# Kernel optimization log

Measured on AMD Instinct MI355X. Metric: run time of the kernel, lower is better.

Reference implementation:

```python
import jax, jax.numpy as jnp
import numpy as np

N, FEAT, D, K, L, H, NCLS = 4096, 512, 64, 100, 3, 8, 2
EPS = 1e-15

def _ln(x, g, b, eps=1e-6):
    m = x.mean(-1, keepdims=True)
    v = x.var(-1, keepdims=True)
    return (x - m) * jax.lax.rsqrt(v + eps) * g + b


def setup_inputs():
    key = jax.random.key(0)
    ks = jax.random.split(key, 12)
    w = lambda k, shape: jax.random.normal(k, shape, jnp.float32) * 0.02
    return {
        "node_feat": jax.random.normal(ks[0], (1, N, FEAT), jnp.float32),
        "adj": jax.random.uniform(ks[1], (1, N, N), jnp.float32),
        "conv_w": w(ks[2], (FEAT, D)), "conv_b": jnp.zeros((D,), jnp.float32),
        "bn_g": jnp.ones((D,), jnp.float32), "bn_b": jnp.zeros((D,), jnp.float32),
        "pool_w": w(ks[3], (D, K)), "pool_b": jnp.zeros((K,), jnp.float32),
        "cls_token": jnp.zeros((1, 1, D), jnp.float32),
        "ln1_g": jnp.ones((L, D), jnp.float32), "ln1_b": jnp.zeros((L, D), jnp.float32),
        "qkv_w": w(ks[4], (L, D, 3 * D)), "qkv_b": jnp.zeros((L, 3 * D), jnp.float32),
        "proj_w": w(ks[5], (L, D, D)), "proj_b": jnp.zeros((L, D), jnp.float32),
        "ln2_g": jnp.ones((L, D), jnp.float32), "ln2_b": jnp.zeros((L, D), jnp.float32),
        "fc1_w": w(ks[6], (L, D, 4 * D)), "fc1_b": jnp.zeros((L, 4 * D), jnp.float32),
        "fc2_w": w(ks[7], (L, 4 * D, D)), "fc2_b": jnp.zeros((L, D), jnp.float32),
        "norm_g": jnp.ones((D,), jnp.float32), "norm_b": jnp.zeros((D,), jnp.float32),
        "head_w": w(ks[8], (D, NCLS)), "head_b": jnp.zeros((NCLS,), jnp.float32),
    }


def _forward(node_feat, adj, conv_w, conv_b, bn_g, bn_b, pool_w, pool_b, cls_token,
             ln1_g, ln1_b, qkv_w, qkv_b, proj_w, proj_b, ln2_g, ln2_b,
             fc1_w, fc1_b, fc2_w, fc2_b, norm_g, norm_b, head_w, head_b):
    x = node_feat  # mask is all ones -> X = mask*X is a no-op
    # --- GCNBlock: propagate + self loop + linear + BatchNorm(train stats) + L2 norm ---
    y = jnp.matmul(adj, x) + x                 # [1,N,F]
    y = y @ conv_w + conv_b                    # [1,N,D]
    m = y.mean(axis=(0, 1))
    v = y.var(axis=(0, 1))
    y = (y - m) * jax.lax.rsqrt(v + 1e-5) * bn_g + bn_b
    y = y / jnp.maximum(jnp.linalg.norm(y, axis=2, keepdims=True), 1e-12)
    # --- cluster assignment ---
    s = jax.nn.softmax(y @ pool_w + pool_b, axis=-1)   # [1,N,K]
    # --- dense_mincut_pool ---
    out = jnp.einsum('bnk,bnd->bkd', s, y)             # [1,K,D]
    sa = s[0].T @ adj[0]                               # [K,N] (the torch.sparse.mm)
    out_adj = (sa @ s[0])[None]                        # [1,K,K]
    mincut_num = jnp.trace(out_adj, axis1=1, axis2=2)  # [1]
    d_flat = adj.sum(-1)                               # [1,N] degrees
    # trace(S^T diag(d) S) = sum_i d_i * ||s_i||^2
    mincut_den = jnp.sum(d_flat[0] * jnp.sum(s[0] ** 2, axis=-1))[None]
    mincut_loss = jnp.mean(-(mincut_num / mincut_den))
    ss = jnp.einsum('bnk,bnl->bkl', s, s)
    i_s = jnp.eye(K, dtype=ss.dtype)
    ortho_loss = jnp.mean(jnp.linalg.norm(
        ss / jnp.linalg.norm(ss, axis=(-1, -2), keepdims=True) - i_s / jnp.linalg.norm(i_s),
        axis=(-1, -2)))
    ind = jnp.arange(K)
    out_adj = out_adj.at[:, ind, ind].set(0.0)
    dd = jnp.sqrt(out_adj.sum(-1))[:, None] + EPS      # [1,1,K]
    out_adj = out_adj / dd / jnp.swapaxes(dd, 1, 2)    # (returned by pool; unused downstream)
    # --- transformer over [cls] + K cluster tokens ---
    t = jnp.concatenate([jnp.broadcast_to(cls_token, (1, 1, D)), out], axis=1)  # [1,K+1,D]
    hd = D // H
    scale = hd ** -0.5
    for l in range(L):
        h = _ln(t, ln1_g[l], ln1_b[l])
        qkv = h @ qkv_w[l] + qkv_b[l]
        q, k, vv = jnp.split(qkv, 3, axis=-1)
        sp = lambda a: a.reshape(1, -1, H, hd).transpose(0, 2, 1, 3)
        q, k, vv = sp(q), sp(k), sp(vv)
        att = jax.nn.softmax(jnp.einsum('bhqd,bhkd->bhqk', q, k) * scale, axis=-1)
        o = jnp.einsum('bhqk,bhkd->bhqd', att, vv).transpose(0, 2, 1, 3).reshape(1, -1, D)
        t = t + (o @ proj_w[l] + proj_b[l])
        h = _ln(t, ln2_g[l], ln2_b[l])
        t = t + (jax.nn.gelu(h @ fc1_w[l] + fc1_b[l], approximate=False) @ fc2_w[l] + fc2_b[l])
    t = _ln(t, norm_g, norm_b)
    logits = t[:, 0] @ head_w + head_b                 # [1,NCLS]
    return logits, mincut_loss, ortho_loss


def reference(node_feat, adj, conv_w, conv_b, bn_g, bn_b, pool_w, pool_b, cls_token,
              ln1_g, ln1_b, qkv_w, qkv_b, proj_w, proj_b, ln2_g, ln2_b,
              fc1_w, fc1_b, fc2_w, fc2_b, norm_g, norm_b, head_w, head_b):
    return _forward(node_feat, adj, conv_w, conv_b, bn_g, bn_b, pool_w, pool_b, cls_token,
                    ln1_g, ln1_b, qkv_w, qkv_b, proj_w, proj_b, ln2_g, ln2_b,
                    fc1_w, fc1_b, fc2_w, fc2_b, norm_g, norm_b, head_w, head_b)
```

## Files before the change

kernel.cpp:

```cpp
#include <hip/hip_runtime.h>
#include <hip/hip_bf16.h>
#include <math.h>

#define NN   4096
#define FEAT 512
#define DIM  64
#define KC   100
#define LL   3

#define OFF_DFLAT   0
#define OFF_CHSUM   4096
#define OFF_CHSQ    4160
#define OFF_CTR     4224
#define ZERO_FLOATS 4240
#define OFF_XW      4240
#define OFF_YPART   (OFF_XW + NN*DIM)
#define OFF_GPART   (OFF_YPART + 8*NN*DIM)
#define OFF_Y0      (OFF_GPART + 64*128*192)
#define OFF_QKV     (OFF_Y0 + NN*DIM)
#define OFF_SS      (OFF_QKV + 2*101*192)
#define OFF_DENP    (OFF_SS + KC*KC)
#define OFF_NUMP    (OFF_DENP + 1024)
#define OFF_SB16    (OFF_NUMP + 1024)
#define OFF_STB16   (OFF_SB16 + NN*128/2)
#define OFF_YNT16   (OFF_STB16 + NN*128/2)
#define OFF_XWT16   (OFF_YNT16 + NN*DIM/2)

typedef __attribute__((ext_vector_type(8))) short bfrag;
typedef __attribute__((ext_vector_type(4))) float ffrag;

__device__ __forceinline__ unsigned short f2bf(float f) {
    union { float f; unsigned u; } v; v.f = f;
    return (unsigned short)((v.u + 0x7FFFu + ((v.u >> 16) & 1u)) >> 16);
}
__device__ __forceinline__ float bf2f(unsigned short u) {
    union { unsigned u; float f; } v; v.u = (unsigned)u << 16; return v.f;
}
__device__ __forceinline__ unsigned int pk2(float a, float b) {
    __hip_bfloat162 h = __float22bfloat162_rn(make_float2(a, b));
    return *(unsigned int*)&h;
}

__device__ __forceinline__ float wsum(float v) {
#pragma unroll
    for (int o = 32; o > 0; o >>= 1) v += __shfl_xor(v, o, 64);
    return v;
}
__device__ __forceinline__ float wmax(float v) {
#pragma unroll
    for (int o = 32; o > 0; o >>= 1) v = fmaxf(v, __shfl_xor(v, o, 64));
    return v;
}
__device__ __forceinline__ float hsum32(float v) {
#pragma unroll
    for (int o = 16; o > 0; o >>= 1) v += __shfl_xor(v, o, 64);
    return v;
}
__device__ __forceinline__ float hmax32(float v) {
#pragma unroll
    for (int o = 16; o > 0; o >>= 1) v = fmaxf(v, __shfl_xor(v, o, 64));
    return v;
}

__device__ __forceinline__ unsigned rlx_load(const unsigned* p) {
    return __hip_atomic_load(p, __ATOMIC_RELAXED, __HIP_MEMORY_SCOPE_AGENT);
}
__device__ __forceinline__ void rel_add(unsigned* p) {
    __hip_atomic_fetch_add(p, 1u, __ATOMIC_RELEASE, __HIP_MEMORY_SCOPE_AGENT);
}
template <int SLP>
__device__ __forceinline__ void wait_ge(const unsigned* c, unsigned tgt) {
    while (rlx_load(c) < tgt) __builtin_amdgcn_s_sleep(SLP);
    __builtin_amdgcn_fence(__ATOMIC_ACQUIRE, "agent");
}
__device__ __forceinline__ void bar() {
    asm volatile("s_waitcnt lgkmcnt(0)" ::: "memory");
    __builtin_amdgcn_s_barrier();
}
__device__ __forceinline__ void gbar(unsigned* c, unsigned tgt) {
    __syncthreads();
    if (threadIdx.x == 0) {
        rel_add(c);
        wait_ge<4>(c, tgt);
    }
    bar();
}

__global__ __launch_bounds__(256) void xwk(const float* __restrict__ x,
                                           const float* __restrict__ B,
                                           float* __restrict__ xw,
                                           unsigned short* __restrict__ xwT,
                                           float* __restrict__ zws) {
    __shared__ float a_sh[16 * 68];
    __shared__ float b_sh[64 * 68];
    __shared__ unsigned short tl[64 * 17];
    const int t = threadIdx.x, rb = blockIdx.x;
    if (rb < 17) {
        const int zi = rb * 256 + t;
        if (zi < ZERO_FLOATS) zws[zi] = 0.f;
    }
    const int r = t >> 4, cg = (t & 15) * 4;
    float4 acc = make_float4(0.f, 0.f, 0.f, 0.f);
    for (int kt = 0; kt < FEAT; kt += 64) {
        *(float4*)&a_sh[(t >> 4) * 68 + (t & 15) * 4] =
            *(const float4*)(x + (size_t)(rb * 16 + (t >> 4)) * FEAT + kt + (t & 15) * 4);
#pragma unroll
        for (int p = 0; p < 4; ++p) {
            const int idx = t + 256 * p;
            const int kr = idx >> 4, c4 = (idx & 15) * 4;
            *(float4*)&b_sh[kr * 68 + c4] = *(const float4*)(B + (size_t)(kt + kr) * DIM + c4);
        }
        __syncthreads();
#pragma unroll 8
        for (int k = 0; k < 64; ++k) {
            const float av = a_sh[r * 68 + k];
            const float4 bv = *(float4*)&b_sh[k * 68 + cg];
            acc.x += av * bv.x; acc.y += av * bv.y;
            acc.z += av * bv.z; acc.w += av * bv.w;
        }
        __syncthreads();
    }
    *(float4*)&xw[(size_t)(rb * 16 + r) * DIM + cg] = acc;
    tl[(cg + 0) * 17 + r] = f2bf(acc.x);
    tl[(cg + 1) * 17 + r] = f2bf(acc.y);
    tl[(cg + 2) * 17 + r] = f2bf(acc.z);
    tl[(cg + 3) * 17 + r] = f2bf(acc.w);
    __syncthreads();
    const int d = t >> 2, c = (t & 3) * 4;
    ushort4 o;
    o.x = tl[d * 17 + c + 0]; o.y = tl[d * 17 + c + 1];
    o.z = tl[d * 17 + c + 2]; o.w = tl[d * 17 + c + 3];
    *(ushort4*)(xwT + (size_t)d * NN + rb * 16 + c) = o;
}

__global__ __launch_bounds__(256) void gemmA(const float* __restrict__ adj,
                                             const unsigned short* __restrict__ xwT,
                                             float* __restrict__ ypart,
                                             float* __restrict__ dflat) {
    __shared__ __align__(16) unsigned short a_sh[32 * 72];
    __shared__ __align__(16) unsigned short b_sh[64 * 72];
    const int t  = threadIdx.x;
    const int rb = blockIdx.x;
    const int k0 = blockIdx.y * 512;
    const int w = t >> 6, lane = t & 63;
    const int m = lane & 15, q = lane >> 4;
    const int ih = w & 1, jh = w >> 1;
    const int srow = t >> 3, sq = t & 7;
    const int bn = t >> 2, bc = t & 3;
    ffrag acc[2];
    acc[0] = (ffrag){0.f, 0.f, 0.f, 0.f};
    acc[1] = (ffrag){0.f, 0.f, 0.f, 0.f};
    float dacc = 0.f;
    const float* abase = adj + (size_t)(rb * 32 + srow) * NN + k0;
    const unsigned short* bbase = xwT + (size_t)bn * NN + k0;
    for (int kt = 0; kt < 512; kt += 64) {
#pragma unroll
        for (int k = 0; k < 2; ++k) {
            const int p = sq + 8 * k;
            const float4 v = *(const float4*)(abase + kt + 4 * p);
            dacc += v.x + v.y + v.z + v.w;
            *(uint2*)(a_sh + srow * 72 + 4 * p) = make_uint2(pk2(v.x, v.y), pk2(v.z, v.w));
        }
#pragma unroll
        for (int k = 0; k < 2; ++k) {
            const int c2 = bc + 4 * k;
            *(bfrag*)(b_sh + bn * 72 + c2 * 8) = *(const bfrag*)(bbase + kt + c2 * 8);
        }
        __syncthreads();
#pragma unroll
        for (int ks = 0; ks < 2; ++ks) {
            const bfrag af = *(const bfrag*)(a_sh + (ih * 16 + m) * 72 + ks * 32 + q * 8);
#pragma unroll
            for (int jj = 0; jj < 2; ++jj) {
                const bfrag bf = *(const bfrag*)(b_sh + ((jh * 2 + jj) * 16 + m) * 72 + ks * 32 + q * 8);
                acc[jj] = __builtin_amdgcn_mfma_f32_16x16x32_bf16(af, bf, acc[jj], 0, 0, 0);
            }
        }
        __syncthreads();
    }
    float* op = ypart + (size_t)blockIdx.y * NN * DIM;
#pragma unroll
    for (int jj = 0; jj < 2; ++jj)
#pragma unroll
        for (int r = 0; r < 4; ++r)
            op[(size_t)(rb * 32 + ih * 16 + q * 4 + r) * DIM + jh * 32 + jj * 16 + m] = acc[jj][r];
    dacc += __shfl_down(dacc, 1, 64);
    dacc += __shfl_down(dacc, 2, 64);
    dacc += __shfl_down(dacc, 4, 64);
    if (sq == 0) atomicAdd(&dflat[rb * 32 + srow], dacc);
}

__global__ __launch_bounds__(256) void bnstat(const float* __restrict__ ypart,
                                              const float* __restrict__ xw,
                                              const float* __restrict__ conv_b,
                                              float* __restrict__ Y0,
                                              float* __restrict__ chsum,
                                              float* __restrict__ chsq) {
    __shared__ float ssum[64], ssq[64];
    const int t = threadIdx.x;
    if (t < 64) { ssum[t] = 0.f; ssq[t] = 0.f; }
    __syncthreads();
    const int tid = blockIdx.x * 256 + t;
    const size_t e = (size_t)tid * 4;
    const int c0 = (int)(e & 63);
    float4 v = *(const float4*)(xw + e);
#pragma unroll
    for (int s = 0; s < 8; ++s) {
        const float4 u = *(const float4*)(ypart + (size_t)s * NN * DIM + e);
        v.x += u.x; v.y += u.y; v.z += u.z; v.w += u.w;
    }
    const float4 b = *(const float4*)(conv_b + c0);
    v.x += b.x; v.y += b.y; v.z += b.z; v.w += b.w;
    *(float4*)(Y0 + e) = v;
    atomicAdd(&ssum[c0 + 0], v.x); atomicAdd(&ssum[c0 + 1], v.y);
    atomicAdd(&ssum[c0 + 2], v.z); atomicAdd(&ssum[c0 + 3], v.w);
    atomicAdd(&ssq[c0 + 0], v.x * v.x); atomicAdd(&ssq[c0 + 1], v.y * v.y);
    atomicAdd(&ssq[c0 + 2], v.z * v.z); atomicAdd(&ssq[c0 + 3], v.w * v.w);
    __syncthreads();
    if (t < 64) { atomicAdd(&chsum[t], ssum[t]); atomicAdd(&chsq[t], ssq[t]); }
}

__global__ __launch_bounds__(256) void rowsk(const float* __restrict__ Y0,
                                             const float* __restrict__ bn_g,
                                             const float* __restrict__ bn_b,
                                             const float* __restrict__ chsum,
                                             const float* __restrict__ chsq,
                                             const float* __restrict__ pool_w,
                                             const float* __restrict__ pool_b,
                                             const float* __restrict__ dflat,
                                             unsigned short* __restrict__ YnT,
                                             unsigned short* __restrict__ Sb16,
                                             unsigned short* __restrict__ ST,
                                             float* __restrict__ denp) {
    __shared__ float scale_sh[64], shift_sh[64];
    __shared__ float yn_sh[4][64];
    __shared__ float4 pw4[16 * 104];
    __shared__ unsigned short sb_sh[4][128];
    __shared__ float denw[4];
    const int t = threadIdx.x;
    if (t < 64) {
        const float mn  = chsum[t] * (1.f / 4096.f);
        const float var = chsq[t] * (1.f / 4096.f) - mn * mn;
        const float sc  = bn_g[t] * rsqrtf(var + 1e-5f);
        scale_sh[t] = sc;
        shift_sh[t] = bn_b[t] - mn * sc;
    }
    for (int idx = t; idx < 16 * KC; idx += 256) {
        const int dq = idx / KC, k = idx - dq * KC;
        pw4[dq * 104 + k] = make_float4(pool_w[(4 * dq + 0) * KC + k],
                                        pool_w[(4 * dq + 1) * KC + k],
                                        pool_w[(4 * dq + 2) * KC + k],
                                        pool_w[(4 * dq + 3) * KC + k]);
    }
    __syncthreads();
    const int w = t >> 6, lane = t & 63;
    const int row = blockIdx.x * 4 + w;
    float v = Y0[(size_t)row * 64 + lane] * scale_sh[lane] + shift_sh[lane];
    const float nrm = fmaxf(sqrtf(wsum(v * v)), 1e-12f);
    const float yn = v / nrm;
    yn_sh[w][lane] = yn;
    const bool v2 = (lane + 64) < KC;
    const int j2 = v2 ? (lane + 64) : 0;
    float L1 = pool_b[lane];
    float L2 = pool_b[j2];
    __syncthreads();
#pragma unroll
    for (int dq = 0; dq < 16; ++dq) {
        const float4 yv = *(const float4*)&yn_sh[w][4 * dq];
        const float4 w1 = pw4[dq * 104 + lane];
        L1 += yv.x * w1.x + yv.y * w1.y + yv.z * w1.z + yv.w * w1.w;
        const float4 w2 = pw4[dq * 104 + j2];
        L2 += yv.x * w2.x + yv.y * w2.y + yv.z * w2.z + yv.w * w2.w;
    }
    const float mx = wmax(fmaxf(L1, v2 ? L2 : -1e30f));
    const float e1 = expf(L1 - mx);
    const float e2 = v2 ? expf(L2 - mx) : 0.f;
    const float inv = 1.f / wsum(e1 + e2);
    const float s1 = e1 * inv, s2 = e2 * inv;
    const unsigned short b1 = f2bf(s1), b2 = f2bf(s2);
    Sb16[(size_t)row * 128 + lane] = b1;
    Sb16[(size_t)row * 128 + 64 + lane] = b2;
    sb_sh[w][lane] = b1;
    sb_sh[w][64 + lane] = b2;
    const float c = wsum(s1 * s1 + s2 * s2);
    if (lane == 0) denw[w] = dflat[row] * c;
    __syncthreads();
    if (t < 64) {
        ushort4 o;
        o.x = f2bf(yn_sh[0][t]); o.y = f2bf(yn_sh[1][t]);
        o.z = f2bf(yn_sh[2][t]); o.w = f2bf(yn_sh[3][t]);
        *(ushort4*)(YnT + (size_t)t * NN + blockIdx.x * 4) = o;
    } else if (t < 192) {
        const int c2 = t - 64;
        ushort4 o;
        o.x = sb_sh[0][c2]; o.y = sb_sh[1][c2];
        o.z = sb_sh[2][c2]; o.w = sb_sh[3][c2];
        *(ushort4*)(ST + (size_t)c2 * NN + blockIdx.x * 4) = o;
    } else if (t == 192) {
        denp[blockIdx.x] = denw[0] + denw[1] + denw[2] + denw[3];
    }
}

__global__ __launch_bounds__(512) void xform(
        const float* __restrict__ adj,
        const unsigned short* __restrict__ ST,
        const unsigned short* __restrict__ Sb16,
        const unsigned short* __restrict__ YnT,
        float* __restrict__ gpart,
        const float* __restrict__ cls,
        float* __restrict__ ssb,
        float* __restrict__ qkvb,
        const float* __restrict__ g1, const float* __restrict__ b1,
        const float* __restrict__ qw, const float* __restrict__ qb,
        const float* __restrict__ pw, const float* __restrict__ pb,
        const float* __restrict__ g2, const float* __restrict__ b2,
        const float* __restrict__ w1, const float* __restrict__ bb1,
        const float* __restrict__ w2, const float* __restrict__ bb2,
        const float* __restrict__ ng, const float* __restrict__ nb,
        const float* __restrict__ hw, const float* __restrict__ hb,
        const float* __restrict__ denp, float* __restrict__ nump,
        unsigned* __restrict__ ctr,
        float* __restrict__ out) {
    __shared__ __align__(16) float big[13332];
    __shared__ float scsh[8 * 104];
    __shared__ __align__(16) float partf[1056];
    __shared__ float q_l[64], osh[64], h2sh[64], h1sh[64], toksh[64], gsh[256];
    __shared__ float redw8[8];
    float (*part)[132] = (float(*)[132])partf;
    const int t = threadIdx.x, b = blockIdx.x;

    if (b < 101) {
        float4 rqkv[6];
        {
            const float4* s4 = (const float4*)qw;
#pragma unroll
            for (int p = 0; p < 6; ++p) rqkv[p] = s4[t + 512 * p];
        }
        if (b == 0) {
            if (t < 64) toksh[t] = cls[t];
        } else {
            if (t == 0) wait_ge<2>(&ctr[3], 64u);
            bar();
            const int row = b - 1;
            if (t < 384) {
                const int col = t % 192, sg = t / 192;
                float v = 0.f;
                const float* gp = gpart + (size_t)row * 192 + col + (size_t)sg * 32 * 24576;
                for (int s = 0; s < 32; ++s) v += gp[(size_t)s * 24576];
                partf[sg * 192 + col] = v;
            }
            bar();
            if (t < 192) {
                const float v = partf[t] + partf[192 + t];
                if (t < 64) toksh[t] = v;
                else if (t < 164) ssb[row * 100 + (t - 64)] = v;
            }
        }
        bar();
        if (t < 64) {
            const float x = toksh[t];
            const float m = wsum(x) * (1.f / 64.f);
            const float var = wsum(x * x) * (1.f / 64.f) - m * m;
            h1sh[t] = (x - m) * rsqrtf(var + 1e-6f) * g1[t] + b1[t];
        }
        bar();
        for (int l = 0; l < LL; ++l) {
            float* qk = qkvb + (size_t)(l & 1) * (101 * 192);
#pragma unroll
            for (int p = 0; p < 6; ++p) ((float4*)big)[t + 512 * p] = rqkv[p];
            bar();
            if (t < 384) {
                const int o = t % 192, grp = t / 192;
                float a = 0.f;
#pragma unroll 8
                for (int e = grp * 32; e < grp * 32 + 32; ++e)
                    a += h1sh[e] * big[e * 192 + o];
                partf[grp * 192 + o] = a;
            }
            bar();
            if (t < 192)
                qk[b * 192 + t] = qb[l * 192 + t] + partf[t] + partf[192 + t];
            gbar(&ctr[l], 101u);
            float4 rkv[7], rq, rpw[2], rw1a[4];
#pragma unroll
            for (int p = 0; p < 7; ++p) {
                const int idx = t + 512 * p;
                if (idx < 3232)
                    rkv[p] = *(const float4*)(qk + (idx >> 5) * 192 + 64 + (idx & 31) * 4);
            }
            if (t < 16) rq = *(const float4*)(qk + b * 192 + t * 4);
#pragma unroll
            for (int p = 0; p < 2; ++p)
                rpw[p] = ((const float4*)(pw + (size_t)l * 4096))[t + 512 * p];
#pragma unroll
            for (int p = 0; p < 4; ++p) {
                const int idx = t + 512 * p;
                rw1a[p] = *(const float4*)(w1 + (size_t)l * 16384 + (idx >> 5) * 256 + (idx & 31) * 4);
            }
            float t_old = 0.f;
            if (t < 64) t_old = toksh[t];
#pragma unroll
            for (int p = 0; p < 7; ++p) {
                const int idx = t + 512 * p;
                if (idx < 3232) {
                    const int k = idx >> 5, c = idx & 31;
                    *(float4*)&big[k * 132 + c * 4] = rkv[p];
                }
            }
            if (t < 16) *(float4*)&q_l[t * 4] = rq;
            bar();
            const float scale = 0.35355339059327373f;
#pragma unroll
            for (int p = 0; p < 2; ++p) {
                const int idx = t + 512 * p;
                if (idx < 808) {
                    const int h = idx / 101, k = idx - h * 101;
                    float s = 0.f;
#pragma unroll
                    for (int d = 0; d < 8; ++d)
                        s += q_l[h * 8 + d] * big[k * 132 + h * 8 + d];
                    scsh[h * 104 + k] = s * scale;
                }
            }
            bar();
            if (t < 256) {
                const int w = t >> 6;
                const int h = w * 2 + ((t >> 5) & 1);
                const int lft = t & 31;
                float v[4];
#pragma unroll
                for (int g = 0; g < 4; ++g) {
                    const int k = lft + 32 * g;
                    v[g] = (k < 101) ? scsh[h * 104 + k] : -1e30f;
                }
                float mm = fmaxf(fmaxf(v[0], v[1]), fmaxf(v[2], v[3]));
                mm = hmax32(mm);
                float s = 0.f;
#pragma unroll
                for (int g = 0; g < 4; ++g) { v[g] = expf(v[g] - mm); s += v[g]; }
                s = hsum32(s);
                const float inv = 1.f / s;
#pragma unroll
                for (int g = 0; g < 4; ++g) {
                    const int k = lft + 32 * g;
                    if (k < 101) scsh[h * 104 + k] = v[g] * inv;
                }
            }
            bar();
            {
                const int o = t & 63, grp = t >> 6;
                float po = 0.f;
                for (int k = grp; k < 101; k += 8)
                    po += scsh[(o >> 3) * 104 + k] * big[k * 132 + 64 + o];
                part[grp][o] = po;
            }
            bar();
            if (t < 64)
                osh[t] = part[0][t] + part[1][t] + part[2][t] + part[3][t]
                       + part[4][t] + part[5][t] + part[6][t] + part[7][t];
            float4 rw1b[4], rw2a[4], rw2b[4];
#pragma unroll
            for (int p = 0; p < 4; ++p) {
                const int idx = t + 512 * p;
                rw1b[p] = *(const float4*)(w1 + (size_t)l * 16384 + (idx >> 5) * 256 + 128 + (idx & 31) * 4);
                rw2a[p] = ((const float4*)(w2 + (size_t)l * 16384))[idx];
                rw2b[p] = ((const float4*)(w2 + (size_t)l * 16384 + 8192))[idx];
            }
            bar();
#pragma unroll
            for (int p = 0; p < 2; ++p) ((float4*)big)[t + 512 * p] = rpw[p];
            bar();
            {
                const int o = t & 63, grp = t >> 6;
                float pp = 0.f;
#pragma unroll
                for (int e = grp * 8; e < grp * 8 + 8; ++e)
                    pp += osh[e] * big[e * 64 + o];
                part[grp][o] = pp;
            }
            bar();
            float t1 = 0.f;
            if (t < 64) {
                float pr = pb[l * 64 + t];
#pragma unroll
                for (int g = 0; g < 8; ++g) pr += part[g][t];
                t1 = t_old + pr;
                const float m = wsum(t1) * (1.f / 64.f);
                const float var = wsum(t1 * t1) * (1.f / 64.f) - m * m;
                h2sh[t] = (t1 - m) * rsqrtf(var + 1e-6f) * g2[l * 64 + t] + b2[l * 64 + t];
            }
            bar();
#pragma unroll
            for (int p = 0; p < 4; ++p) {
                const int idx = t + 512 * p;
                *(float4*)&big[(idx >> 5) * 128 + (idx & 31) * 4] = rw1a[p];
            }
            bar();
            {
                const int o = t & 127, grp = t >> 7;
                float pa = 0.f;
#pragma unroll
                for (int e = grp * 16; e < grp * 16 + 16; ++e)
                    pa += h2sh[e] * big[e * 128 + o];
                part[grp][o] = pa;
            }
            bar();
            if (t < 128) {
                float a = bb1[l * 256 + t]
                        + part[0][t] + part[1][t] + part[2][t] + part[3][t];
                gsh[t] = 0.5f * a * (1.f + erff(a * 0.70710678118654752f));
            }
            bar();
#pragma unroll
            for (int p = 0; p < 4; ++p) {
                const int idx = t + 512 * p;
                *(float4*)&big[(idx >> 5) * 128 + (idx & 31) * 4] = rw1b[p];
            }
            bar();
            {
                const int o = t & 127, grp = t >> 7;
                float pa = 0.f;
#pragma unroll
                for (int e = grp * 16; e < grp * 16 + 16; ++e)
                    pa += h2sh[e] * big[e * 128 + o];
                part[grp][o] = pa;
            }
            bar();
            if (t < 128) {
                float a = bb1[l * 256 + 128 + t]
                        + part[0][t] + part[1][t] + part[2][t] + part[3][t];
                gsh[128 + t] = 0.5f * a * (1.f + erff(a * 0.70710678118654752f));
            }
            bar();
            float a2p = 0.f;
#pragma unroll
            for (int p = 0; p < 4; ++p) ((float4*)big)[t + 512 * p] = rw2a[p];
            bar();
            {
                const int o = t & 63, grp = t >> 6;
#pragma unroll
                for (int er = grp * 16; er < grp * 16 + 16; ++er)
                    a2p += gsh[er] * big[er * 64 + o];
            }
            bar();
#pragma unroll
            for (int p = 0; p < 4; ++p) ((float4*)big)[t + 512 * p] = rw2b[p];
            bar();
            {
                const int o = t & 63, grp = t >> 6;
#pragma unroll
                for (int er = grp * 16; er < grp * 16 + 16; ++er)
                    a2p += gsh[128 + er] * big[er * 64 + o];
            }
            if (l < 2) {
                const float4* s4 = (const float4*)(qw + (size_t)(l + 1) * 12288);
#pragma unroll
                for (int p = 0; p < 6; ++p) rqkv[p] = s4[t + 512 * p];
            }
            bar();
            {
                const int o = t & 63, grp = t >> 6;
                part[grp][o] = a2p;
            }
            bar();
            if (t < 64) {
                float a2 = bb2[l * 64 + t];
#pragma unroll
                for (int g = 0; g < 8; ++g) a2 += part[g][t];
                const float tn = t1 + a2;
                toksh[t] = tn;
                if (l < 2) {
                    const float m = wsum(tn) * (1.f / 64.f);
                    const float var = wsum(tn * tn) * (1.f / 64.f) - m * m;
                    h1sh[t] = (tn - m) * rsqrtf(var + 1e-6f) * g1[(l + 1) * 64 + t]
                              + b1[(l + 1) * 64 + t];
                }
            }
            bar();
        }
        if (b == 0) {
            if (t < 64) {
                const float x = toksh[t];
                const float m = wsum(x) * (1.f / 64.f);
                const float var = wsum(x * x) * (1.f / 64.f) - m * m;
                h1sh[t] = (x - m) * rsqrtf(var + 1e-6f) * ng[t] + nb[t];
            }
            if (t == 0) wait_ge<8>(&ctr[4], 155u);
            __syncthreads();
            float* red = partf;
            red[t] = denp[t] + denp[t + 512];
            __syncthreads();
            for (int s = 256; s > 0; s >>= 1) { if (t < s) red[t] += red[t + s]; __syncthreads(); }
            if (t == 0) q_l[0] = red[0];
            __syncthreads();
            red[t] = nump[t] + nump[t + 512];
            __syncthreads();
            for (int s = 256; s > 0; s >>= 1) { if (t < s) red[t] += red[t + s]; __syncthreads(); }
            if (t == 0) q_l[1] = red[0];
            __syncthreads();
            if (t < 2) {
                float a = hb[t];
                for (int d = 0; d < 64; ++d) a += h1sh[d] * hw[d * 2 + t];
                out[t] = a;
            }
            if (t == 2) out[2] = -(q_l[1] / q_l[0]);
            float s1 = 0.f;
            for (int idx = t; idx < KC * KC; idx += 512) { const float v = ssb[idx]; s1 += v * v; }
            __syncthreads();
            red[t] = s1;
            __syncthreads();
            for (int s = 256; s > 0; s >>= 1) { if (t < s) red[t] += red[t + s]; __syncthreads(); }
            if (t == 0) q_l[2] = sqrtf(red[0]);
            __syncthreads();
            const float inv = 1.f / q_l[2];
            float s2 = 0.f;
            for (int idx = t; idx < KC * KC; idx += 512) {
                float v = ssb[idx] * inv;
                if (idx % 101 == 0) v -= 0.1f;
                s2 += v * v;
            }
            __syncthreads();
            red[t] = s2;
            __syncthreads();
            for (int s = 256; s > 0; s >>= 1) { if (t < s) red[t] += red[t + s]; __syncthreads(); }
            if (t == 0) out[3] = sqrtf(red[0]);
        }
    } else {
        const int wb = b - 101;
        const int w = t >> 6, lane = t & 63;
        const int m = lane & 15, q = lane >> 4;
        if (wb < 64) {
            unsigned short* a_sh = (unsigned short*)big;
            unsigned short* b_sh = (unsigned short*)big + 128 * 72;
            const int k0 = wb * 64;
            const int n0 = t >> 3, c8 = (t & 7) * 8;
#pragma unroll
            for (int p = 0; p < 2; ++p) {
                const int n = n0 + 64 * p;
                *(bfrag*)(a_sh + n * 72 + c8) = *(const bfrag*)(ST + (size_t)n * NN + k0 + c8);
            }
#pragma unroll
            for (int p = 0; p < 3; ++p) {
                const int n = n0 + 64 * p;
                const unsigned short* src = (n < 64) ? (YnT + (size_t)n * NN + k0 + c8)
                                                     : (ST + (size_t)(n - 64) * NN + k0 + c8);
                *(bfrag*)(b_sh + n * 72 + c8) = *(const bfrag*)src;
            }
            __syncthreads();
            ffrag acc[12];
#pragma unroll
            for (int j = 0; j < 12; ++j) acc[j] = (ffrag){0.f, 0.f, 0.f, 0.f};
#pragma unroll
            for (int ks = 0; ks < 2; ++ks) {
                const bfrag af = *(const bfrag*)(a_sh + (w * 16 + m) * 72 + ks * 32 + q * 8);
#pragma unroll
                for (int j = 0; j < 12; ++j) {
                    const bfrag bf = *(const bfrag*)(b_sh + (j * 16 + m) * 72 + ks * 32 + q * 8);
                    acc[j] = __builtin_amdgcn_mfma_f32_16x16x32_bf16(af, bf, acc[j], 0, 0, 0);
                }
            }
            float* op = gpart + (size_t)wb * 128 * 192;
#pragma unroll
            for (int j = 0; j < 12; ++j)
#pragma unroll
                for (int r = 0; r < 4; ++r)
                    op[(size_t)(w * 16 + q * 4 + r) * 192 + j * 16 + m] = acc[j][r];
            __syncthreads();
            if (t == 0) rel_add(&ctr[3]);
        }
        unsigned short* a_sh = (unsigned short*)big;
        unsigned short* s_sh = (unsigned short*)big + 32 * 72;
        const int rh = w & 1, ch = w >> 1;
        const int srow = t >> 4, sq4 = (t & 15) * 4;
        const int sn = t >> 2, scq = t & 3;
        for (int tile = wb; tile < 1024; tile += 155) {
            const int rb = tile & 127;
            const int k0 = (tile >> 7) * 512;
            ffrag acc[2];
            acc[0] = (ffrag){0.f, 0.f, 0.f, 0.f};
            acc[1] = (ffrag){0.f, 0.f, 0.f, 0.f};
            const float* abase = adj + (size_t)(rb * 32 + srow) * NN + k0;
            const unsigned short* sbase = ST + (size_t)sn * NN + k0;
            for (int kt = 0; kt < 512; kt += 64) {
                {
                    const float4 v = *(const float4*)(abase + kt + sq4);
                    *(uint2*)(a_sh + srow * 72 + sq4) = make_uint2(pk2(v.x, v.y), pk2(v.z, v.w));
                }
#pragma unroll
                for (int k = 0; k < 2; ++k) {
                    const int c2 = scq + 4 * k;
                    *(bfrag*)(s_sh + sn * 72 + c2 * 8) = *(const bfrag*)(sbase + kt + c2 * 8);
                }
                __syncthreads();
#pragma unroll
                for (int ks = 0; ks < 2; ++ks) {
                    const bfrag af = *(const bfrag*)(a_sh + (rh * 16 + m) * 72 + ks * 32 + q * 8);
#pragma unroll
                    for (int j = 0; j < 2; ++j) {
                        const bfrag bf = *(const bfrag*)(s_sh + ((ch * 2 + j) * 16 + m) * 72 + ks * 32 + q * 8);
                        acc[j] = __builtin_amdgcn_mfma_f32_16x16x32_bf16(af, bf, acc[j], 0, 0, 0);
                    }
                }
                __syncthreads();
            }
            float local = 0.f;
#pragma unroll
            for (int j = 0; j < 2; ++j)
#pragma unroll
                for (int r = 0; r < 4; ++r) {
                    const int row = rb * 32 + rh * 16 + q * 4 + r;
                    const int col = ch * 32 + j * 16 + m;
                    local += acc[j][r] * bf2f(Sb16[(size_t)row * 128 + col]);
                }
            local = wsum(local);
            if (lane == 0) redw8[w] = local;
            __syncthreads();
            if (t == 0) {
                float s = 0.f;
#pragma unroll
                for (int k = 0; k < 8; ++k) s += redw8[k];
                nump[(tile >> 7) * 128 + rb] = s;
            }
            __syncthreads();
        }
        __syncthreads();
        if (t == 0) rel_add(&ctr[4]);
    }
}

extern "C" void kernel_launch(void* const* d_in, const int* in_sizes, int n_in,
                              void* d_out, int out_size, void* d_ws, size_t ws_size,
                              hipStream_t stream) {
    (void)in_sizes; (void)n_in; (void)out_size; (void)ws_size;
    const float* x      = (const float*)d_in[0];
    const float* adj    = (const float*)d_in[1];
    const float* conv_w = (const float*)d_in[2];
    const float* conv_b = (const float*)d_in[3];
    const float* bn_g   = (const float*)d_in[4];
    const float* bn_b   = (const float*)d_in[5];
    const float* pool_w = (const float*)d_in[6];
    const float* pool_b = (const float*)d_in[7];
    const float* cls    = (const float*)d_in[8];
    const float* ln1_g  = (const float*)d_in[9];
    const float* ln1_b  = (const float*)d_in[10];
    const float* qkv_w  = (const float*)d_in[11];
    const float* qkv_b  = (const float*)d_in[12];
    const float* proj_w = (const float*)d_in[13];
    const float* proj_b = (const float*)d_in[14];
    const float* ln2_g  = (const float*)d_in[15];
    const float* ln2_b  = (const float*)d_in[16];
    const float* fc1_w  = (const float*)d_in[17];
    const float* fc1_b  = (const float*)d_in[18];
    const float* fc2_w  = (const float*)d_in[19];
    const float* fc2_b  = (const float*)d_in[20];
    const float* norm_g = (const float*)d_in[21];
    const float* norm_b = (const float*)d_in[22];
    const float* head_w = (const float*)d_in[23];
    const float* head_b = (const float*)d_in[24];
    float* ws  = (float*)d_ws;
    float* out = (float*)d_out;
    unsigned short* Sb16  = (unsigned short*)(ws + OFF_SB16);
    unsigned short* STb16 = (unsigned short*)(ws + OFF_STB16);
    unsigned short* YnT16 = (unsigned short*)(ws + OFF_YNT16);
    unsigned short* xwT16 = (unsigned short*)(ws + OFF_XWT16);

    xwk<<<256, 256, 0, stream>>>(x, conv_w, ws + OFF_XW, xwT16, ws);
    gemmA<<<dim3(128, 8), 256, 0, stream>>>(adj, xwT16, ws + OFF_YPART, ws + OFF_DFLAT);
    bnstat<<<256, 256, 0, stream>>>(ws + OFF_YPART, ws + OFF_XW, conv_b,
                                    ws + OFF_Y0, ws + OFF_CHSUM, ws + OFF_CHSQ);
    rowsk<<<1024, 256, 0, stream>>>(ws + OFF_Y0, bn_g, bn_b, ws + OFF_CHSUM, ws + OFF_CHSQ,
                                    pool_w, pool_b, ws + OFF_DFLAT,
                                    YnT16, Sb16, STb16, ws + OFF_DENP);
    xform<<<256, 512, 0, stream>>>(adj, STb16, Sb16, YnT16, ws + OFF_GPART, cls,
                                   ws + OFF_SS, ws + OFF_QKV,
                                   ln1_g, ln1_b, qkv_w, qkv_b, proj_w, proj_b,
                                   ln2_g, ln2_b, fc1_w, fc1_b, fc2_w, fc2_b,
                                   norm_g, norm_b, head_w, head_b,
                                   ws + OFF_DENP, ws + OFF_NUMP,
                                   (unsigned*)(ws + OFF_CTR), out);
}
```

Baseline: 290.3 us.

## Software-pipeline adj/ST tile loads and reschedule weight prefetches in xform

Register double-buffering is added to the adj·S tile loop: the next k-slice of adj and ST is loaded while the current slice is in LDS and feeding the MFMAs. Transformer-layer weight prefetches (proj, fc1, fc2, next qkv) are moved closer to where they are used, which cuts peak register pressure, and one barrier in the fc2 phase is dropped. Launch bounds are set to one block per SM, some __syncthreads are replaced with a cheaper LDS-only barrier, and an extra vmcnt wait is added after the grid-barrier spin. The trade-off is less prefetch distance for the weights and possible race risk from the removed barriers.

After: 281.1 us. 1.03x faster.

```diff
diff --git a/kernel.cpp b/kernel.cpp
--- a/kernel.cpp
+++ b/kernel.cpp
@@ -72,6 +72,7 @@
 __device__ __forceinline__ void wait_ge(const unsigned* c, unsigned tgt) {
     while (rlx_load(c) < tgt) __builtin_amdgcn_s_sleep(SLP);
     __builtin_amdgcn_fence(__ATOMIC_ACQUIRE, "agent");
+    asm volatile("s_waitcnt vmcnt(0)" ::: "memory");
 }
 __device__ __forceinline__ void bar() {
     asm volatile("s_waitcnt lgkmcnt(0)" ::: "memory");
@@ -301,7 +302,7 @@
     }
 }
 
-__global__ __launch_bounds__(512) void xform(
+__global__ __launch_bounds__(512, 1) void xform(
         const float* __restrict__ adj,
         const unsigned short* __restrict__ ST,
         const unsigned short* __restrict__ Sb16,
@@ -381,7 +382,7 @@
             if (t < 192)
                 qk[b * 192 + t] = qb[l * 192 + t] + partf[t] + partf[192 + t];
             gbar(&ctr[l], 101u);
-            float4 rkv[7], rq, rpw[2], rw1a[4];
+            float4 rkv[7], rq;
 #pragma unroll
             for (int p = 0; p < 7; ++p) {
                 const int idx = t + 512 * p;
@@ -389,14 +390,6 @@
                     rkv[p] = *(const float4*)(qk + (idx >> 5) * 192 + 64 + (idx & 31) * 4);
             }
             if (t < 16) rq = *(const float4*)(qk + b * 192 + t * 4);
-#pragma unroll
-            for (int p = 0; p < 2; ++p)
-                rpw[p] = ((const float4*)(pw + (size_t)l * 4096))[t + 512 * p];
-#pragma unroll
-            for (int p = 0; p < 4; ++p) {
-                const int idx = t + 512 * p;
-                rw1a[p] = *(const float4*)(w1 + (size_t)l * 16384 + (idx >> 5) * 256 + (idx & 31) * 4);
-            }
             float t_old = 0.f;
             if (t < 64) t_old = toksh[t];
 #pragma unroll
@@ -408,6 +401,10 @@
                 }
             }
             if (t < 16) *(float4*)&q_l[t * 4] = rq;
+            float4 rpw[2];
+#pragma unroll
+            for (int p = 0; p < 2; ++p)
+                rpw[p] = ((const float4*)(pw + (size_t)l * 4096))[t + 512 * p];
             bar();
             const float scale = 0.35355339059327373f;
 #pragma unroll
@@ -458,13 +455,11 @@
             if (t < 64)
                 osh[t] = part[0][t] + part[1][t] + part[2][t] + part[3][t]
                        + part[4][t] + part[5][t] + part[6][t] + part[7][t];
-            float4 rw1b[4], rw2a[4], rw2b[4];
+            float4 rw1a[4];
 #pragma unroll
             for (int p = 0; p < 4; ++p) {
                 const int idx = t + 512 * p;
-                rw1b[p] = *(const float4*)(w1 + (size_t)l * 16384 + (idx >> 5) * 256 + 128 + (idx & 31) * 4);
-                rw2a[p] = ((const float4*)(w2 + (size_t)l * 16384))[idx];
-                rw2b[p] = ((const float4*)(w2 + (size_t)l * 16384 + 8192))[idx];
+                rw1a[p] = *(const float4*)(w1 + (size_t)l * 16384 + (idx >> 5) * 256 + (idx & 31) * 4);
             }
             bar();
 #pragma unroll
@@ -489,6 +484,12 @@
                 const float var = wsum(t1 * t1) * (1.f / 64.f) - m * m;
                 h2sh[t] = (t1 - m) * rsqrtf(var + 1e-6f) * g2[l * 64 + t] + b2[l * 64 + t];
             }
+            float4 rw1b[4];
+#pragma unroll
+            for (int p = 0; p < 4; ++p) {
+                const int idx = t + 512 * p;
+                rw1b[p] = *(const float4*)(w1 + (size_t)l * 16384 + (idx >> 5) * 256 + 128 + (idx & 31) * 4);
+            }
             bar();
 #pragma unroll
             for (int p = 0; p < 4; ++p) {
@@ -510,6 +511,10 @@
                         + part[0][t] + part[1][t] + part[2][t] + part[3][t];
                 gsh[t] = 0.5f * a * (1.f + erff(a * 0.70710678118654752f));
             }
+            float4 rw2a[4];
+#pragma unroll
+            for (int p = 0; p < 4; ++p)
+                rw2a[p] = ((const float4*)(w2 + (size_t)l * 16384))[t + 512 * p];
             bar();
 #pragma unroll
             for (int p = 0; p < 4; ++p) {
@@ -531,6 +536,10 @@
                         + part[0][t] + part[1][t] + part[2][t] + part[3][t];
                 gsh[128 + t] = 0.5f * a * (1.f + erff(a * 0.70710678118654752f));
             }
+            float4 rw2b[4];
+#pragma unroll
+            for (int p = 0; p < 4; ++p)
+                rw2b[p] = ((const float4*)(w2 + (size_t)l * 16384 + 8192))[t + 512 * p];
             bar();
             float a2p = 0.f;
 #pragma unroll
@@ -542,6 +551,11 @@
                 for (int er = grp * 16; er < grp * 16 + 16; ++er)
                     a2p += gsh[er] * big[er * 64 + o];
             }
+            if (l < 2) {
+                const float4* s4 = (const float4*)(qw + (size_t)(l + 1) * 12288);
+#pragma unroll
+                for (int p = 0; p < 6; ++p) rqkv[p] = s4[t + 512 * p];
+            }
             bar();
 #pragma unroll
             for (int p = 0; p < 4; ++p) ((float4*)big)[t + 512 * p] = rw2b[p];
@@ -552,12 +566,6 @@
                 for (int er = grp * 16; er < grp * 16 + 16; ++er)
                     a2p += gsh[128 + er] * big[er * 64 + o];
             }
-            if (l < 2) {
-                const float4* s4 = (const float4*)(qw + (size_t)(l + 1) * 12288);
-#pragma unroll
-                for (int p = 0; p < 6; ++p) rqkv[p] = s4[t + 512 * p];
-            }
-            bar();
             {
                 const int o = t & 63, grp = t >> 6;
                 part[grp][o] = a2p;
@@ -681,17 +689,20 @@
             acc[1] = (ffrag){0.f, 0.f, 0.f, 0.f};
             const float* abase = adj + (size_t)(rb * 32 + srow) * NN + k0;
             const unsigned short* sbase = ST + (size_t)sn * NN + k0;
+            float4 av = *(const float4*)(abase + sq4);
+            bfrag sv0 = *(const bfrag*)(sbase + scq * 8);
+            bfrag sv1 = *(const bfrag*)(sbase + (scq + 4) * 8);
+#pragma unroll
             for (int kt = 0; kt < 512; kt += 64) {
-                {
-                    const float4 v = *(const float4*)(abase + kt + sq4);
-                    *(uint2*)(a_sh + srow * 72 + sq4) = make_uint2(pk2(v.x, v.y), pk2(v.z, v.w));
-                }
-#pragma unroll
-                for (int k = 0; k < 2; ++k) {
-                    const int c2 = scq + 4 * k;
-                    *(bfrag*)(s_sh + sn * 72 + c2 * 8) = *(const bfrag*)(sbase + kt + c2 * 8);
-                }
-                __syncthreads();
+                *(uint2*)(a_sh + srow * 72 + sq4) = make_uint2(pk2(av.x, av.y), pk2(av.z, av.w));
+                *(bfrag*)(s_sh + sn * 72 + scq * 8) = sv0;
+                *(bfrag*)(s_sh + sn * 72 + (scq + 4) * 8) = sv1;
+                if (kt + 64 < 512) {
+                    av  = *(const float4*)(abase + kt + 64 + sq4);
+                    sv0 = *(const bfrag*)(sbase + kt + 64 + scq * 8);
+                    sv1 = *(const bfrag*)(sbase + kt + 64 + (scq + 4) * 8);
+                }
+                bar();
 #pragma unroll
                 for (int ks = 0; ks < 2; ++ks) {
                     const bfrag af = *(const bfrag*)(a_sh + (rh * 16 + m) * 72 + ks * 32 + q * 8);
@@ -701,7 +712,7 @@
                         acc[j] = __builtin_amdgcn_mfma_f32_16x16x32_bf16(af, bf, acc[j], 0, 0, 0);
                     }
                 }
-                __syncthreads();
+                bar();
             }
             float local = 0.f;
 #pragma unroll
@@ -714,14 +725,13 @@
                 }
             local = wsum(local);
             if (lane == 0) redw8[w] = local;
-            __syncthreads();
+            bar();
             if (t == 0) {
                 float s = 0.f;
 #pragma unroll
                 for (int k = 0; k < 8; ++k) s += redw8[k];
                 nump[(tile >> 7) * 128 + rb] = s;
             }
-            __syncthreads();
         }
         __syncthreads();
         if (t == 0) rel_add(&ctr[4]);
```
